# Performance work log

Hardware: AMD Instinct MI355X
Metric: run time of the kernel (lower is better)

The kernel has to match this reference:

```python
import jax, jax.numpy as jnp
import numpy as np

EPS = 1e-8
NS = 1e9  # nanoseconds per second


def qmult(a, b):
    aw, ax, ay, az = a[..., 0], a[..., 1], a[..., 2], a[..., 3]
    bw, bx, by, bz = b[..., 0], b[..., 1], b[..., 2], b[..., 3]
    return jnp.stack([
        aw * bw - ax * bx - ay * by - az * bz,
        aw * bx + ax * bw + ay * bz - az * by,
        aw * by - ax * bz + ay * bw + az * bx,
        aw * bz + ax * by - ay * bx + az * bw,
    ], axis=-1)


def qinv(q):
    # unit-quaternion inverse == conjugate
    return q * jnp.array([1.0, -1.0, -1.0, -1.0], dtype=q.dtype)


def qexp(v):
    # log-quaternion (..., 3) -> unit quaternion (..., 4)
    n = jnp.maximum(jnp.linalg.norm(v, axis=-1, keepdims=True), EPS)
    return jnp.concatenate([jnp.cos(n), jnp.sin(n) / n * v], axis=-1)


def qlog(q):
    # unit quaternion (..., 4) -> log-quaternion (..., 3)
    n = jnp.maximum(jnp.linalg.norm(q[..., 1:], axis=-1, keepdims=True), EPS)
    return q[..., 1:] * jnp.arccos(jnp.clip(q[..., :1], -1.0, 1.0)) / n


def rotate_vec(v, q):
    # rotate vector v (..., 3) by quaternion q (..., 4)
    vq = jnp.concatenate([jnp.zeros_like(v[..., :1]), v], axis=-1)
    return qmult(qmult(q, vq), qinv(q))[..., 1:]


def l1(a, b):
    return jnp.mean(jnp.abs(a - b))


def setup_inputs() -> dict:
    key = jax.random.key(0)
    k1, k2, k3 = jax.random.split(key, 3)
    N, T = 2048, 1024
    pred = jax.random.normal(k1, (N, T, 6), dtype=jnp.float32)
    targ = jax.random.normal(k2, (N, T, 6), dtype=jnp.float32)
    imu = jax.random.normal(k3, (N, T, 10), dtype=jnp.float32)
    ts = jnp.broadcast_to(jnp.arange(T, dtype=jnp.float32) * 5e6, (N, T))
    imu = imu.at[..., 9].set(ts)
    z = jnp.zeros((1,), dtype=jnp.float32)
    return {"pred": pred, "targ": targ, "imu": imu,
            "sax": z, "saq": z, "srx": z, "srq": z}


def reference(pred, targ, imu, sax, saq, srx, srq):
    # ---- absolute pose loss ----
    abs_loss = (jnp.exp(-sax) * l1(pred[..., :3], targ[..., :3]) + sax
                + jnp.exp(-saq) * l1(pred[..., 3:], targ[..., 3:]) + saq)

    # ---- simple VOs: consecutive differences (N, T-1, 6) ----
    pred_vos = pred[:, 1:] - pred[:, :-1]
    targ_vos = targ[:, 1:] - targ[:, :-1]

    # ---- true relative poses from targ (calc_vos) ----
    q0 = qexp(targ[:, :-1, 3:])            # (N, T-1, 4)
    q1 = qexp(targ[:, 1:, 3:])
    q0i = qinv(q0)
    targ_imu_q = qlog(qmult(q0i, q1))      # (N, T-1, 3) rotation part of calc_vos

    # ---- IMU integration (vectorized over the original N x T python loop) ----
    ts = imu[..., 9]
    dt = ((ts[:, 1:] - ts[:, :-1]) / NS)[..., None]   # (N, T-1, 1) seconds
    accel = imu[:, :-1, 0:3]
    vel = imu[:, :-1, 3:6]
    ang_vel = imu[:, :-1, 6:9]
    imu_trans = vel * dt + 0.5 * accel * dt * dt       # (N, T-1, 3)

    wnorm = jnp.maximum(jnp.linalg.norm(ang_vel, axis=-1, keepdims=True), EPS)
    theta = wnorm * dt                                  # rotation angle over dt
    dq = jnp.concatenate([jnp.cos(0.5 * theta),
                          (ang_vel / wnorm) * jnp.sin(0.5 * theta)], axis=-1)
    new_q = jax.lax.stop_gradient(qmult(q0, dq))        # numpy round-trip in torch detaches
    imu_ori_shift = qlog(qmult(q0i, new_q))             # (N, T-1, 3)

    # ---- relative (VO) loss ----
    vo_loss = (jnp.exp(-srx) * l1(pred_vos[..., :3], targ_vos[..., :3]) + srx
               + jnp.exp(-srq) * l1(pred_vos[..., 3:], targ_vos[..., 3:]) + srq)

    # ---- IMU loss ----
    imu_loss = (jnp.exp(-srx) * l1(pred_vos[..., :3], imu_trans) + srx
                + jnp.exp(-srq) * l1(targ_imu_q, imu_ori_shift) + srq)

    return abs_loss + vo_loss + imu_loss   # shape (1,)
```

## Files before the change

kernel.cpp:

```cpp
#include <hip/hip_runtime.h>
#include <math.h>

#define NN 2048
#define TT 1024
#define EPSF 1e-8f

#define GRID   2048
#define BLOCK  256
#define STRIDE (GRID * BLOCK)
#define ITER   ((NN * TT) / STRIDE)

struct Quat { float w, x, y, z; };

__device__ inline Quat qmul(const Quat a, const Quat b) {
    Quat r;
    r.w = a.w * b.w - a.x * b.x - a.y * b.y - a.z * b.z;
    r.x = a.w * b.x + a.x * b.w + a.y * b.z - a.z * b.y;
    r.y = a.w * b.y - a.x * b.z + a.y * b.w + a.z * b.x;
    r.z = a.w * b.z + a.x * b.y - a.y * b.x + a.z * b.w;
    return r;
}

__device__ inline Quat qexp3(float vx, float vy, float vz) {
    float n = fmaxf(sqrtf(vx * vx + vy * vy + vz * vz), EPSF);
    float s = __sinf(n) / n;
    Quat r;
    r.w = __cosf(n);
    r.x = s * vx; r.y = s * vy; r.z = s * vz;
    return r;
}

__device__ inline void qlog3(const Quat q, float& ox, float& oy, float& oz) {
    float n = fmaxf(sqrtf(q.x * q.x + q.y * q.y + q.z * q.z), EPSF);
    float c = fminf(fmaxf(q.w, -1.0f), 1.0f);
    float s = acosf(c) / n;
    ox = q.x * s; oy = q.y * s; oz = q.z * s;
}

__device__ inline float waveReduceF(float v) {
    #pragma unroll
    for (int o = 32; o > 0; o >>= 1) v += __shfl_down(v, o);
    return v;
}

__device__ inline double waveReduceD(double v) {
    #pragma unroll
    for (int o = 32; o > 0; o >>= 1) v += __shfl_down(v, o);
    return v;
}

__global__ __launch_bounds__(BLOCK) void loss_main(
    const float* __restrict__ pred, const float* __restrict__ targ,
    const float* __restrict__ imu, float* __restrict__ partial)
{
    float s0 = 0.f, s1 = 0.f, s2 = 0.f, s3 = 0.f, s4 = 0.f, s5 = 0.f;
    const int base = blockIdx.x * BLOCK + threadIdx.x;

    #pragma unroll
    for (int k = 0; k < ITER; ++k) {
        const int idx = base + k * STRIDE;
        const int t = idx & (TT - 1);
        const float2* pr = reinterpret_cast<const float2*>(pred) + (size_t)idx * 3;
        const float2* tg = reinterpret_cast<const float2*>(targ) + (size_t)idx * 3;
        float2 p0 = pr[0], p1 = pr[1], p2 = pr[2];
        float2 g0 = tg[0], g1 = tg[1], g2 = tg[2];

        s0 += fabsf(p0.x - g0.x) + fabsf(p0.y - g0.y) + fabsf(p1.x - g1.x);
        s1 += fabsf(p1.y - g1.y) + fabsf(p2.x - g2.x) + fabsf(p2.y - g2.y);

        if (t < TT - 1) {
            float2 n0 = pr[3], n1 = pr[4], n2 = pr[5];
            float2 h0 = tg[3], h1 = tg[4], h2 = tg[5];

            float pv0 = n0.x - p0.x, pv1 = n0.y - p0.y, pv2 = n1.x - p1.x;
            float pv3 = n1.y - p1.y, pv4 = n2.x - p2.x, pv5 = n2.y - p2.y;
            float tv0 = h0.x - g0.x, tv1 = h0.y - g0.y, tv2 = h1.x - g1.x;
            float tv3 = h1.y - g1.y, tv4 = h2.x - g2.x, tv5 = h2.y - g2.y;

            s2 += fabsf(pv0 - tv0) + fabsf(pv1 - tv1) + fabsf(pv2 - tv2);
            s3 += fabsf(pv3 - tv3) + fabsf(pv4 - tv4) + fabsf(pv5 - tv5);

            Quat q0 = qexp3(g1.y, g2.x, g2.y);
            Quat q1 = qexp3(h1.y, h2.x, h2.y);
            Quat q0i; q0i.w = q0.w; q0i.x = -q0.x; q0i.y = -q0.y; q0i.z = -q0.z;
            Quat r01 = qmul(q0i, q1);
            float tq0, tq1, tq2;
            qlog3(r01, tq0, tq1, tq2);

            const float2* im = reinterpret_cast<const float2*>(imu) + (size_t)idx * 5;
            float2 i0 = im[0], i1 = im[1], i2 = im[2], i3 = im[3], i4 = im[4];
            float ts0 = i4.y;
            float ts1 = im[9].y;
            float dt = (ts1 - ts0) * 1e-9f;

            float a0 = i0.x, a1 = i0.y, a2 = i1.x;
            float v0 = i1.y, v1 = i2.x, v2 = i2.y;
            float w0 = i3.x, w1 = i3.y, w2 = i4.x;

            float hdt2 = 0.5f * dt * dt;
            float it0 = v0 * dt + a0 * hdt2;
            float it1 = v1 * dt + a1 * hdt2;
            float it2 = v2 * dt + a2 * hdt2;
            s4 += fabsf(pv0 - it0) + fabsf(pv1 - it1) + fabsf(pv2 - it2);

            float wn = fmaxf(sqrtf(w0 * w0 + w1 * w1 + w2 * w2), EPSF);
            float half = 0.5f * wn * dt;
            float sd = __sinf(half) / wn;
            Quat dq; dq.w = __cosf(half); dq.x = w0 * sd; dq.y = w1 * sd; dq.z = w2 * sd;
            Quat nq = qmul(q0, dq);
            Quat m  = qmul(q0i, nq);
            float io0, io1, io2;
            qlog3(m, io0, io1, io2);
            s5 += fabsf(tq0 - io0) + fabsf(tq1 - io1) + fabsf(tq2 - io2);
        }
    }

    s0 = waveReduceF(s0); s1 = waveReduceF(s1); s2 = waveReduceF(s2);
    s3 = waveReduceF(s3); s4 = waveReduceF(s4); s5 = waveReduceF(s5);

    __shared__ float red[4][6];
    const int lane = threadIdx.x & 63;
    const int wid  = threadIdx.x >> 6;
    if (lane == 0) {
        red[wid][0] = s0; red[wid][1] = s1; red[wid][2] = s2;
        red[wid][3] = s3; red[wid][4] = s4; red[wid][5] = s5;
    }
    __syncthreads();
    if (threadIdx.x < 6) {
        const int c = threadIdx.x;
        partial[(size_t)blockIdx.x * 6 + c] = red[0][c] + red[1][c] + red[2][c] + red[3][c];
    }
}

__global__ __launch_bounds__(256) void loss_finalize(
    const float* __restrict__ partial,
    const float* __restrict__ sax, const float* __restrict__ saq,
    const float* __restrict__ srx, const float* __restrict__ srq,
    float* __restrict__ out)
{
    double t0 = 0, t1 = 0, t2 = 0, t3 = 0, t4 = 0, t5 = 0;
    for (int r = threadIdx.x; r < GRID; r += 256) {
        const float* p = partial + (size_t)r * 6;
        t0 += p[0]; t1 += p[1]; t2 += p[2];
        t3 += p[3]; t4 += p[4]; t5 += p[5];
    }
    t0 = waveReduceD(t0); t1 = waveReduceD(t1); t2 = waveReduceD(t2);
    t3 = waveReduceD(t3); t4 = waveReduceD(t4); t5 = waveReduceD(t5);

    __shared__ double red[4][6];
    const int lane = threadIdx.x & 63;
    const int wid  = threadIdx.x >> 6;
    if (lane == 0) {
        red[wid][0] = t0; red[wid][1] = t1; red[wid][2] = t2;
        red[wid][3] = t3; red[wid][4] = t4; red[wid][5] = t5;
    }
    __syncthreads();
    if (threadIdx.x == 0) {
        double a0 = 0, a1 = 0, a2 = 0, a3 = 0, a4 = 0, a5 = 0;
        #pragma unroll
        for (int w = 0; w < 4; ++w) {
            a0 += red[w][0]; a1 += red[w][1]; a2 += red[w][2];
            a3 += red[w][3]; a4 += red[w][4]; a5 += red[w][5];
        }
        const double inv_abs = 1.0 / ((double)NN * TT * 3);
        const double inv_vo  = 1.0 / ((double)NN * (TT - 1) * 3);
        float A = (float)(a0 * inv_abs);
        float B = (float)(a1 * inv_abs);
        float C = (float)(a2 * inv_vo);
        float D = (float)(a3 * inv_vo);
        float E = (float)(a4 * inv_vo);
        float F = (float)(a5 * inv_vo);
        float sx = sax[0], sq = saq[0], rx = srx[0], rq = srq[0];
        out[0] = expf(-sx) * A + sx + expf(-sq) * B + sq
               + expf(-rx) * (C + E) + 2.0f * rx
               + expf(-rq) * (D + F) + 2.0f * rq;
    }
}

extern "C" void kernel_launch(void* const* d_in, const int* in_sizes, int n_in,
                              void* d_out, int out_size, void* d_ws, size_t ws_size,
                              hipStream_t stream) {
    const float* pred = (const float*)d_in[0];
    const float* targ = (const float*)d_in[1];
    const float* imu  = (const float*)d_in[2];
    const float* sax  = (const float*)d_in[3];
    const float* saq  = (const float*)d_in[4];
    const float* srx  = (const float*)d_in[5];
    const float* srq  = (const float*)d_in[6];
    float* out = (float*)d_out;
    float* partial = (float*)d_ws;

    loss_main<<<GRID, BLOCK, 0, stream>>>(pred, targ, imu, partial);
    loss_finalize<<<1, 256, 0, stream>>>(partial, sax, saq, srx, srq, out);
}
```

Measured before the change: 207.4 us.

## Process two timesteps per thread with float4 loads and shared quaternion exp

Each thread now handles a pair of consecutive timesteps, loading pred, targ and imu as float4 vectors instead of float2. The middle quaternion exp is computed once and reused by both difference terms, and only the small next-step element is fetched as an extra load. This cuts redundant neighbour reloads and transcendental work per element. The cost is higher register pressure and some unaligned scalar and float2 tail loads.

```diff
diff --git a/kernel.cpp b/kernel.cpp
--- a/kernel.cpp
+++ b/kernel.cpp
@@ -5,10 +5,12 @@
 #define TT 1024
 #define EPSF 1e-8f
 
-#define GRID   2048
-#define BLOCK  256
-#define STRIDE (GRID * BLOCK)
-#define ITER   ((NN * TT) / STRIDE)
+#define BLOCK    256
+#define GRID     2048
+#define NPAIR    (NN * TT / 2)
+#define NTHREADS (GRID * BLOCK)
+#define PITER    (NPAIR / NTHREADS)
+#define PAIRS_PER_N (TT / 2)
 
 struct Quat { float w, x, y, z; };
 
@@ -21,6 +23,10 @@
     return r;
 }
 
+__device__ inline Quat qconj(const Quat q) {
+    Quat r; r.w = q.w; r.x = -q.x; r.y = -q.y; r.z = -q.z; return r;
+}
+
 __device__ inline Quat qexp3(float vx, float vy, float vz) {
     float n = fmaxf(sqrtf(vx * vx + vy * vy + vz * vz), EPSF);
     float s = __sinf(n) / n;
@@ -49,6 +55,44 @@
     return v;
 }
 
+__device__ inline void pair_terms(
+    const float pa[6], const float pb[6], const float ga[6], const float gb[6],
+    const Quat qR, const Quat qN,
+    float a0, float a1, float a2, float v0, float v1, float v2,
+    float w0, float w1, float w2, float ts0, float ts1,
+    float& s2, float& s3, float& s4, float& s5)
+{
+    float pv0 = pb[0] - pa[0], pv1 = pb[1] - pa[1], pv2 = pb[2] - pa[2];
+    float pv3 = pb[3] - pa[3], pv4 = pb[4] - pa[4], pv5 = pb[5] - pa[5];
+    float tv0 = gb[0] - ga[0], tv1 = gb[1] - ga[1], tv2 = gb[2] - ga[2];
+    float tv3 = gb[3] - ga[3], tv4 = gb[4] - ga[4], tv5 = gb[5] - ga[5];
+
+    s2 += fabsf(pv0 - tv0) + fabsf(pv1 - tv1) + fabsf(pv2 - tv2);
+    s3 += fabsf(pv3 - tv3) + fabsf(pv4 - tv4) + fabsf(pv5 - tv5);
+
+    Quat qRi = qconj(qR);
+    Quat r01 = qmul(qRi, qN);
+    float tq0, tq1, tq2;
+    qlog3(r01, tq0, tq1, tq2);
+
+    float dt = (ts1 - ts0) * 1e-9f;
+    float hdt2 = 0.5f * dt * dt;
+    float it0 = v0 * dt + a0 * hdt2;
+    float it1 = v1 * dt + a1 * hdt2;
+    float it2 = v2 * dt + a2 * hdt2;
+    s4 += fabsf(pv0 - it0) + fabsf(pv1 - it1) + fabsf(pv2 - it2);
+
+    float wn = fmaxf(sqrtf(w0 * w0 + w1 * w1 + w2 * w2), EPSF);
+    float half = 0.5f * wn * dt;
+    float sd = __sinf(half) / wn;
+    Quat dq; dq.w = __cosf(half); dq.x = w0 * sd; dq.y = w1 * sd; dq.z = w2 * sd;
+    Quat nq = qmul(qR, dq);
+    Quat m  = qmul(qRi, nq);
+    float io0, io1, io2;
+    qlog3(m, io0, io1, io2);
+    s5 += fabsf(tq0 - io0) + fabsf(tq1 - io1) + fabsf(tq2 - io2);
+}
+
 __global__ __launch_bounds__(BLOCK) void loss_main(
     const float* __restrict__ pred, const float* __restrict__ targ,
     const float* __restrict__ imu, float* __restrict__ partial)
@@ -57,61 +101,56 @@
     const int base = blockIdx.x * BLOCK + threadIdx.x;
 
     #pragma unroll
-    for (int k = 0; k < ITER; ++k) {
-        const int idx = base + k * STRIDE;
-        const int t = idx & (TT - 1);
-        const float2* pr = reinterpret_cast<const float2*>(pred) + (size_t)idx * 3;
-        const float2* tg = reinterpret_cast<const float2*>(targ) + (size_t)idx * 3;
-        float2 p0 = pr[0], p1 = pr[1], p2 = pr[2];
-        float2 g0 = tg[0], g1 = tg[1], g2 = tg[2];
-
-        s0 += fabsf(p0.x - g0.x) + fabsf(p0.y - g0.y) + fabsf(p1.x - g1.x);
-        s1 += fabsf(p1.y - g1.y) + fabsf(p2.x - g2.x) + fabsf(p2.y - g2.y);
-
-        if (t < TT - 1) {
-            float2 n0 = pr[3], n1 = pr[4], n2 = pr[5];
-            float2 h0 = tg[3], h1 = tg[4], h2 = tg[5];
-
-            float pv0 = n0.x - p0.x, pv1 = n0.y - p0.y, pv2 = n1.x - p1.x;
-            float pv3 = n1.y - p1.y, pv4 = n2.x - p2.x, pv5 = n2.y - p2.y;
-            float tv0 = h0.x - g0.x, tv1 = h0.y - g0.y, tv2 = h1.x - g1.x;
-            float tv3 = h1.y - g1.y, tv4 = h2.x - g2.x, tv5 = h2.y - g2.y;
-
-            s2 += fabsf(pv0 - tv0) + fabsf(pv1 - tv1) + fabsf(pv2 - tv2);
-            s3 += fabsf(pv3 - tv3) + fabsf(pv4 - tv4) + fabsf(pv5 - tv5);
-
-            Quat q0 = qexp3(g1.y, g2.x, g2.y);
-            Quat q1 = qexp3(h1.y, h2.x, h2.y);
-            Quat q0i; q0i.w = q0.w; q0i.x = -q0.x; q0i.y = -q0.y; q0i.z = -q0.z;
-            Quat r01 = qmul(q0i, q1);
-            float tq0, tq1, tq2;
-            qlog3(r01, tq0, tq1, tq2);
-
-            const float2* im = reinterpret_cast<const float2*>(imu) + (size_t)idx * 5;
-            float2 i0 = im[0], i1 = im[1], i2 = im[2], i3 = im[3], i4 = im[4];
-            float ts0 = i4.y;
-            float ts1 = im[9].y;
-            float dt = (ts1 - ts0) * 1e-9f;
-
-            float a0 = i0.x, a1 = i0.y, a2 = i1.x;
-            float v0 = i1.y, v1 = i2.x, v2 = i2.y;
-            float w0 = i3.x, w1 = i3.y, w2 = i4.x;
-
-            float hdt2 = 0.5f * dt * dt;
-            float it0 = v0 * dt + a0 * hdt2;
-            float it1 = v1 * dt + a1 * hdt2;
-            float it2 = v2 * dt + a2 * hdt2;
-            s4 += fabsf(pv0 - it0) + fabsf(pv1 - it1) + fabsf(pv2 - it2);
-
-            float wn = fmaxf(sqrtf(w0 * w0 + w1 * w1 + w2 * w2), EPSF);
-            float half = 0.5f * wn * dt;
-            float sd = __sinf(half) / wn;
-            Quat dq; dq.w = __cosf(half); dq.x = w0 * sd; dq.y = w1 * sd; dq.z = w2 * sd;
-            Quat nq = qmul(q0, dq);
-            Quat m  = qmul(q0i, nq);
-            float io0, io1, io2;
-            qlog3(m, io0, io1, io2);
-            s5 += fabsf(tq0 - io0) + fabsf(tq1 - io1) + fabsf(tq2 - io2);
+    for (int k = 0; k < PITER; ++k) {
+        const int u = base + k * NTHREADS;
+        const int tp = u & (PAIRS_PER_N - 1);
+
+        const float4* p4 = reinterpret_cast<const float4*>(pred) + (size_t)u * 3;
+        const float4* g4 = reinterpret_cast<const float4*>(targ) + (size_t)u * 3;
+        const float4* i4 = reinterpret_cast<const float4*>(imu)  + (size_t)u * 5;
+
+        float4 P0 = p4[0], P1 = p4[1], P2 = p4[2];
+        float4 G0 = g4[0], G1 = g4[1], G2 = g4[2];
+        float4 I0 = i4[0], I1 = i4[1], I2 = i4[2], I3 = i4[3], I4 = i4[4];
+
+        float pA[6] = {P0.x, P0.y, P0.z, P0.w, P1.x, P1.y};
+        float pB[6] = {P1.z, P1.w, P2.x, P2.y, P2.z, P2.w};
+        float gA[6] = {G0.x, G0.y, G0.z, G0.w, G1.x, G1.y};
+        float gB[6] = {G1.z, G1.w, G2.x, G2.y, G2.z, G2.w};
+
+        s0 += fabsf(pA[0]-gA[0]) + fabsf(pA[1]-gA[1]) + fabsf(pA[2]-gA[2])
+            + fabsf(pB[0]-gB[0]) + fabsf(pB[1]-gB[1]) + fabsf(pB[2]-gB[2]);
+        s1 += fabsf(pA[3]-gA[3]) + fabsf(pA[4]-gA[4]) + fabsf(pA[5]-gA[5])
+            + fabsf(pB[3]-gB[3]) + fabsf(pB[4]-gB[4]) + fabsf(pB[5]-gB[5]);
+
+        Quat qA = qexp3(gA[3], gA[4], gA[5]);
+        Quat qB = qexp3(gB[3], gB[4], gB[5]);
+
+        float tsA = I2.y, tsB = I4.w;
+
+        pair_terms(pA, pB, gA, gB, qA, qB,
+                   I0.x, I0.y, I0.z,
+                   I0.w, I1.x, I1.y,
+                   I1.z, I1.w, I2.x,
+                   tsA, tsB, s2, s3, s4, s5);
+
+        if (tp != PAIRS_PER_N - 1) {
+            float4 P3 = p4[3];
+            float2 PF = reinterpret_cast<const float2*>(pred)[(size_t)u * 6 + 8];
+            float4 G3 = g4[3];
+            float2 GF = reinterpret_cast<const float2*>(targ)[(size_t)u * 6 + 8];
+            float tsC = imu[(size_t)u * 20 + 29];
+
+            float pC[6] = {P3.x, P3.y, P3.z, P3.w, PF.x, PF.y};
+            float gC[6] = {G3.x, G3.y, G3.z, G3.w, GF.x, GF.y};
+
+            Quat qC = qexp3(gC[3], gC[4], gC[5]);
+
+            pair_terms(pB, pC, gB, gC, qB, qC,
+                       I2.z, I2.w, I3.x,
+                       I3.y, I3.z, I3.w,
+                       I4.x, I4.y, I4.z,
+                       tsB, tsC, s2, s3, s4, s5);
         }
     }
 
```

Result: no change. 209.9 us (+1.2%).
